# Performance work log

Hardware: AMD Instinct MI355X
Metric: run time of the kernel (lower is better)

The kernel has to match this reference:

```python
import jax, jax.numpy as jnp
import numpy as np
from jax import lax

B, T, H, W, C = 2, 16, 64, 64, 64
KT, K = 3, 3


def kernel_to_freq_3d(kernel, T, H, W):
    # kernel: (C, k_t, k_h, k_w) -> (C, T, H, W) complex freq response
    Cc, k_t, k_h, k_w = kernel.shape
    t_idx = (jnp.arange(k_t) - k_t // 2) % T
    h_idx = (jnp.arange(k_h) - k_h // 2) % H
    w_idx = (jnp.arange(k_w) - k_w // 2) % W
    tt, th, tw = jnp.meshgrid(t_idx, h_idx, w_idx, indexing='ij')
    padded = jnp.zeros((Cc, T, H, W), dtype=kernel.dtype).at[:, tt, th, tw].set(kernel)
    return jnp.fft.fftn(padded, axes=(1, 2, 3))


def mamba_op(left, right):
    a1, b1 = left
    a2, b2 = right
    return (a1 * a2, a2 * b1 + b2)


def setup_inputs() -> dict:
    key = jax.random.key(0)
    ks = jax.random.split(key, 8)
    fan_in = KT * K * K
    x = jax.random.normal(ks[0], (B, T, H, W, C), dtype=jnp.float32)
    A_kernel = jax.random.normal(ks[1], (C, KT, K, K), dtype=jnp.float32) / np.sqrt(fan_in)
    B_kernel = jax.random.normal(ks[2], (C, KT, K, K), dtype=jnp.float32) / np.sqrt(fan_in)
    forget_bias = jnp.full((C,), 2.0, dtype=jnp.float32)
    forget_scale = jnp.full((C,), 0.01, dtype=jnp.float32)
    input_bias = jnp.zeros((C,), dtype=jnp.float32)
    input_scale = jnp.full((C,), 0.01, dtype=jnp.float32)
    delta_W = jax.random.normal(ks[3], (C, C), dtype=jnp.float32) / np.sqrt(C)
    delta_b = jnp.zeros((C,), dtype=jnp.float32)
    return {"x": x, "A_kernel": A_kernel, "B_kernel": B_kernel,
            "forget_bias": forget_bias, "forget_scale": forget_scale,
            "input_bias": input_bias, "input_scale": input_scale,
            "delta_W": delta_W, "delta_b": delta_b}


def reference(x, A_kernel, B_kernel, forget_bias, forget_scale,
              input_bias, input_scale, delta_W, delta_b):
    Bb, Tt, Hh, Ww, Cc = x.shape
    # freq-domain kernels: (C,T,H,W) -> (T,1,H,W,C) for broadcasting over batch
    A_f = kernel_to_freq_3d(A_kernel, Tt, Hh, Ww).transpose(1, 2, 3, 0)[:, None]
    B_f = kernel_to_freq_3d(B_kernel, Tt, Hh, Ww).transpose(1, 2, 3, 0)[:, None]
    # input-dependent gates (real, elementwise per channel)
    forget_gate = jax.nn.sigmoid(forget_bias + forget_scale * x)
    input_gate = jax.nn.sigmoid(input_bias + input_scale * x)
    delta = jax.nn.softplus(jnp.einsum('bthwc,cd->bthwd', x, delta_W) + delta_b)
    x_f = jnp.fft.fftn(x, axes=(1, 2, 3))  # complex (B,T,H,W,C)
    # move time axis to front for the scan: (T,B,H,W,C)
    a_seq = forget_gate.transpose(1, 0, 2, 3, 4) * A_f
    b_seq = (input_gate.transpose(1, 0, 2, 3, 4)
             * delta.transpose(1, 0, 2, 3, 4)
             * B_f * x_f.transpose(1, 0, 2, 3, 4))
    _, h_all_f = lax.associative_scan(mamba_op, (a_seq, b_seq), axis=0)
    h_f = h_all_f.transpose(1, 0, 2, 3, 4)
    h = jnp.fft.ifftn(h_f, axes=(1, 2, 3)).real
    return h.astype(x.dtype)
```

## Files before the change

kernel.cpp:

```cpp
#include <hip/hip_runtime.h>
#include <math.h>

#define Bb 2
#define Tt 16
#define Hh 64
#define Ww 64
#define Cc 64
#define ST_ (Hh*Ww*Cc)
#define SB_ (Tt*Hh*Ww*Cc)

#define TWO_PI 6.2831853071795864769f

typedef __attribute__((ext_vector_type(8))) short bf16x8;
typedef __attribute__((ext_vector_type(4))) float f32x4;

#define BUF_A    0u
#define BUF_B    8388608u

__device__ __forceinline__ float2 cmul(float2 a, float2 b) {
    return make_float2(fmaf(a.x, b.x, -a.y * b.y), fmaf(a.x, b.y, a.y * b.x));
}
__device__ __forceinline__ float2 cadd(float2 a, float2 b) { return make_float2(a.x + b.x, a.y + b.y); }
__device__ __forceinline__ float2 csub(float2 a, float2 b) { return make_float2(a.x - b.x, a.y - b.y); }

__device__ __forceinline__ unsigned bfpack(float2 f) {
    unsigned r = __float_as_uint(f.x);
    unsigned i = __float_as_uint(f.y);
    r = (r + 0x7fffu + ((r >> 16) & 1u)) >> 16;
    i = (i + 0x7fffu + ((i >> 16) & 1u)) >> 16;
    return r | (i << 16);
}
__device__ __forceinline__ float2 bfunpack(unsigned u) {
    return make_float2(__uint_as_float(u << 16), __uint_as_float(u & 0xffff0000u));
}

union U48 { uint4 u4; uint2 u2[2]; unsigned u[4]; bf16x8 v8; };

__device__ __forceinline__ U48 tw_wf(int wp, int q, int ka, int reim) {
    U48 o;
#pragma unroll
    for (int p = 0; p < 4; ++p) {
        int k0 = ka * 32 + q * 8 + 2 * p;
        float v[2];
#pragma unroll
        for (int dk = 0; dk < 2; ++dk) {
            int k = k0 + dk;
            int a = (wp * k) & 63;
            float sn, cs; sincosf(TWO_PI * (float)a * (1.0f / 64.0f), &sn, &cs);
            v[dk] = reim ? -sn : cs;
        }
        o.u[p] = bfpack(make_float2(v[0], v[1]));
    }
    return o;
}

__device__ __forceinline__ U48 tw_cpx(int wp, int q, int ka, int reim, int tbl) {
    U48 o;
#pragma unroll
    for (int p = 0; p < 4; ++p) {
        int k0 = ka * 32 + q * 8 + 2 * p;
        float v[2];
#pragma unroll
        for (int dk = 0; dk < 2; ++dk) {
            int k = k0 + dk;
            int h = k >> 1;
            int a = (wp * h) & 63;
            float sn, cs; sincosf(TWO_PI * (float)a * (1.0f / 64.0f), &sn, &cs);
            bool even = (k & 1) == 0;
            float vv;
            if (tbl == 1) vv = reim ? (even ? -sn : cs) : (even ? cs : sn);
            else          vv = (reim ? (even ? sn : cs) : (even ? cs : -sn)) * (1.0f / 64.0f);
            v[dk] = vv;
        }
        o.u[p] = bfpack(make_float2(v[0], v[1]));
    }
    return o;
}

__device__ __forceinline__ U48 tw_wi(int wp, int q, int ka) {
    U48 o;
#pragma unroll
    for (int p = 0; p < 4; ++p) {
        int k0 = ka * 32 + q * 8 + 2 * p;
        float v[2];
#pragma unroll
        for (int dk = 0; dk < 2; ++dk) {
            int k = k0 + dk;
            int h = k >> 1;
            int a = (wp * h) & 63;
            float sn, cs; sincosf(TWO_PI * (float)a * (1.0f / 64.0f), &sn, &cs);
            bool even = (k & 1) == 0;
            v[dk] = (even ? cs : -sn) * (1.0f / 64.0f);
        }
        o.u[p] = bfpack(make_float2(v[0], v[1]));
    }
    return o;
}

__device__ __forceinline__ int zidx(int col, int h) {
    return (col << 6) + (h ^ (((col >> 1) & 7) << 3));
}

template <int S>
__device__ __forceinline__ void fft4(float2& a, float2& b, float2& c, float2& d) {
    float2 t0 = cadd(a, c), t1 = csub(a, c);
    float2 t2 = cadd(b, d), t3 = csub(b, d);
    a = cadd(t0, t2);
    c = csub(t0, t2);
    b = make_float2(t1.x - (float)S * t3.y, t1.y + (float)S * t3.x);
    d = make_float2(t1.x + (float)S * t3.y, t1.y - (float)S * t3.x);
}

template <int S>
__device__ __forceinline__ void fft16(float2 v[16]) {
    const float CS[10] = {1.f, 0.92387953f, 0.70710678f, 0.38268343f, 0.f,
                          -0.38268343f, -0.70710678f, -0.92387953f, -1.f, -0.92387953f};
    const float SN[10] = {0.f, 0.38268343f, 0.70710678f, 0.92387953f, 1.f,
                          0.92387953f, 0.70710678f, 0.38268343f, 0.f, -0.38268343f};
    float2 A[4][4];
#pragma unroll
    for (int j = 0; j < 4; ++j) {
        A[j][0] = v[j]; A[j][1] = v[4 + j]; A[j][2] = v[8 + j]; A[j][3] = v[12 + j];
        fft4<S>(A[j][0], A[j][1], A[j][2], A[j][3]);
#pragma unroll
        for (int k0 = 0; k0 < 4; ++k0) {
            int m = j * k0;
            float2 tw = make_float2(CS[m], (float)S * SN[m]);
            A[j][k0] = cmul(A[j][k0], tw);
        }
    }
#pragma unroll
    for (int k0 = 0; k0 < 4; ++k0) {
        fft4<S>(A[0][k0], A[1][k0], A[2][k0], A[3][k0]);
        v[k0] = A[0][k0]; v[k0 + 4] = A[1][k0]; v[k0 + 8] = A[2][k0]; v[k0 + 12] = A[3][k0];
    }
}

__global__ __launch_bounds__(512) void k_fwd2d(const float* __restrict__ x,
                                               unsigned* __restrict__ X2) {
    __shared__ unsigned Z[512 * 64];
    __shared__ unsigned P[8 * 16 * 32];
    int tid = threadIdx.x;
    int lane = tid & 63, r = (tid >> 6) & 3, team = tid >> 8;
    int wv = tid >> 6;
    int m = lane & 15, q = lane >> 4;
    int wg = blockIdx.x;
    int bt = wg >> 3;
    int c0 = (wg & 7) * 8;
    int b = wg >> 7, t = (wg >> 3) & 15;
    const float* xs = x + (size_t)bt * 262144;
    int wp = r * 16 + m;
    int hme = m >> 3, cme = m & 7;

    U48 Are[2], Aim[2];
#pragma unroll
    for (int ka = 0; ka < 2; ++ka) { Are[ka] = tw_wf(wp, q, ka, 0); Aim[ka] = tw_wf(wp, q, ka, 1); }

    int s_hl = lane >> 4;
    int s_p  = (lane >> 1) & 7;
    int s_cq = lane & 1;
    int s_hb = wv & 3;
    int s_wh = wv >> 2;

    for (int ch = 0; ch < 4; ++ch) {
        int hloc = s_hb * 4 + s_hl;
        int h = ch * 16 + hloc;
#pragma unroll
        for (int st = 0; st < 2; ++st) {
            int w2 = s_wh * 16 + st * 8 + s_p;
            const float* pa = xs + (size_t)h * 4096 + (size_t)w2 * 128 + (c0 + s_cq * 4);
            float4 f0 = *(const float4*)pa;
            float4 f1 = *(const float4*)(pa + 64);
            float a0[4] = {f0.x, f0.y, f0.z, f0.w};
            float a1[4] = {f1.x, f1.y, f1.z, f1.w};
            int hb3 = h & 3;
#pragma unroll
            for (int j = 0; j < 4; ++j) {
                int c = s_cq * 4 + j;
                int w2s = w2 ^ ((hb3 ^ ((c & 1) << 1)) << 3);
                P[c * 512 + hloc * 32 + w2s] = bfpack(make_float2(a0[j], a1[j]));
            }
        }
        __syncthreads();
#pragma unroll
        for (int gi = 0; gi < 4; ++gi) {
            int g = ch * 8 + gi * 2 + team;
            int h2 = g * 2 + hme;
            int hl2 = h2 & 15;
            int swz = ((h2 & 3) ^ ((cme & 1) << 1)) << 3;
            U48 B[2];
#pragma unroll
            for (int ka = 0; ka < 2; ++ka) {
                int w2a = (ka * 16 + q * 4) ^ swz;
                B[ka].u4 = *(const uint4*)&P[cme * 512 + hl2 * 32 + w2a];
            }
            f32x4 ar = {0.f, 0.f, 0.f, 0.f}, ai = {0.f, 0.f, 0.f, 0.f};
#pragma unroll
            for (int ka = 0; ka < 2; ++ka) {
                ar = __builtin_amdgcn_mfma_f32_16x16x32_bf16(Are[ka].v8, B[ka].v8, ar, 0, 0, 0);
                ai = __builtin_amdgcn_mfma_f32_16x16x32_bf16(Aim[ka].v8, B[ka].v8, ai, 0, 0, 0);
            }
#pragma unroll
            for (int reg = 0; reg < 4; ++reg) {
                int wpp = r * 16 + q * 4 + reg;
                Z[zidx(wpp * 8 + cme, h2)] = bfpack(make_float2(ar[reg], ai[reg]));
            }
        }
        __syncthreads();
    }

    U48 Hre[4], Him[4];
#pragma unroll
    for (int ka = 0; ka < 4; ++ka) { Hre[ka] = tw_cpx(wp, q, ka, 0, 1); Him[ka] = tw_cpx(wp, q, ka, 1, 1); }
    size_t ob = (size_t)b * 4194304 + (size_t)t * 64 + (c0 + cme);
#pragma unroll 2
    for (int gi = 0; gi < 16; ++gi) {
        int g = gi * 2 + team;
        int col = g * 16 + m;
        int w = g * 2 + hme;
        U48 B[4];
#pragma unroll
        for (int ka = 0; ka < 4; ++ka) {
            int h0 = ka * 16 + q * 4;
            int zi = zidx(col, h0);
            B[ka].u2[0] = *(const uint2*)&Z[zi];
            B[ka].u2[1] = *(const uint2*)&Z[zi + 2];
        }
        f32x4 ar = {0.f, 0.f, 0.f, 0.f}, ai = {0.f, 0.f, 0.f, 0.f};
#pragma unroll
        for (int ka = 0; ka < 4; ++ka) {
            ar = __builtin_amdgcn_mfma_f32_16x16x32_bf16(Hre[ka].v8, B[ka].v8, ar, 0, 0, 0);
            ai = __builtin_amdgcn_mfma_f32_16x16x32_bf16(Him[ka].v8, B[ka].v8, ai, 0, 0, 0);
        }
#pragma unroll
        for (int reg = 0; reg < 4; ++reg) {
            int hp = r * 16 + q * 4 + reg;
            X2[ob + (size_t)hp * 65536 + (size_t)w * 1024] = bfpack(make_float2(ar[reg], ai[reg]));
        }
    }
}

__global__ __launch_bounds__(512) void k_inv2d(const unsigned* __restrict__ X3,
                                               float* __restrict__ out) {
    __shared__ unsigned Z[512 * 64];
    __shared__ unsigned P[8 * 8 * 64];
    int tid = threadIdx.x;
    int lane = tid & 63, r = (tid >> 6) & 3, team = tid >> 8;
    int m = lane & 15, q = lane >> 4;
    int wg = blockIdx.x;
    int bt = wg >> 3;
    int c0 = (wg & 7) * 8;
    const unsigned* xs = X3 + (size_t)bt * 262144;
    int wp = r * 16 + m;
    int hme = m >> 3, cme = m & 7;

    U48 Hre[4], Him[4];
#pragma unroll
    for (int ka = 0; ka < 4; ++ka) { Hre[ka] = tw_cpx(wp, q, ka, 0, 2); Him[ka] = tw_cpx(wp, q, ka, 1, 2); }

    for (int cw = 0; cw < 8; ++cw) {
#pragma unroll
        for (int it = 0; it < 2; ++it) {
            int u = it * 512 + tid;
            int cq = u & 1, h = (u >> 1) & 63, wl = u >> 7;
            const unsigned* pa = xs + (size_t)(cw * 8 + wl) * 4096 + (size_t)h * 64 + (c0 + cq * 4);
            uint4 d = *(const uint4*)pa;
            unsigned dd[4] = {d.x, d.y, d.z, d.w};
#pragma unroll
            for (int j = 0; j < 4; ++j) {
                int c = cq * 4 + j;
                int hs = h ^ ((((wl & 3) ^ ((c & 1) << 1))) << 3);
                P[c * 512 + wl * 64 + hs] = dd[j];
            }
        }
        __syncthreads();
#pragma unroll
        for (int gi = 0; gi < 2; ++gi) {
            int g = cw * 4 + gi * 2 + team;
            int w = g * 2 + hme;
            int wl = w & 7;
            int swz = ((wl & 3) ^ ((cme & 1) << 1)) << 3;
            U48 B[4];
#pragma unroll
            for (int ka = 0; ka < 4; ++ka) {
                int ha = (ka * 16 + q * 4) ^ swz;
                B[ka].u4 = *(const uint4*)&P[cme * 512 + wl * 64 + ha];
            }
            f32x4 ar = {0.f, 0.f, 0.f, 0.f}, ai = {0.f, 0.f, 0.f, 0.f};
#pragma unroll
            for (int ka = 0; ka < 4; ++ka) {
                ar = __builtin_amdgcn_mfma_f32_16x16x32_bf16(Hre[ka].v8, B[ka].v8, ar, 0, 0, 0);
                ai = __builtin_amdgcn_mfma_f32_16x16x32_bf16(Him[ka].v8, B[ka].v8, ai, 0, 0, 0);
            }
#pragma unroll
            for (int reg = 0; reg < 4; ++reg) {
                int hp = r * 16 + q * 4 + reg;
                Z[zidx(hp * 8 + cme, w)] = bfpack(make_float2(ar[reg], ai[reg]));
            }
        }
        __syncthreads();
    }

    U48 Wre[4];
#pragma unroll
    for (int ka = 0; ka < 4; ++ka) Wre[ka] = tw_wi(wp, q, ka);
#pragma unroll 2
    for (int gi = 0; gi < 16; ++gi) {
        int g = gi * 2 + team;
        int col = g * 16 + m;
        int h = g * 2 + hme;
        U48 B[4];
#pragma unroll
        for (int ka = 0; ka < 4; ++ka) {
            int w0 = ka * 16 + q * 4;
            int zi = zidx(col, w0);
            B[ka].u2[0] = *(const uint2*)&Z[zi];
            B[ka].u2[1] = *(const uint2*)&Z[zi + 2];
        }
        f32x4 ar = {0.f, 0.f, 0.f, 0.f};
#pragma unroll
        for (int ka = 0; ka < 4; ++ka)
            ar = __builtin_amdgcn_mfma_f32_16x16x32_bf16(Wre[ka].v8, B[ka].v8, ar, 0, 0, 0);
        float* dst = out + (size_t)bt * 262144 + (size_t)h * 4096 + (c0 + cme);
#pragma unroll
        for (int reg = 0; reg < 4; ++reg) {
            int wpp = r * 16 + q * 4 + reg;
            dst[(size_t)wpp * 64] = ar[reg];
        }
    }
}

__global__ __launch_bounds__(256) void k_mid(
    const float* __restrict__ x, const unsigned* __restrict__ X2,
    unsigned* __restrict__ X3,
    const float* __restrict__ Ak, const float* __restrict__ Bk,
    const float* __restrict__ fb, const float* __restrict__ fs,
    const float* __restrict__ ib, const float* __restrict__ isc_,
    const float* __restrict__ dW, const float* __restrict__ db) {
    const float CT[16] = {1.f, 0.9238795f, 0.7071068f, 0.3826834f, 0.f, -0.3826834f,
                          -0.7071068f, -0.9238795f, -1.f, -0.9238795f, -0.7071068f,
                          -0.3826834f, 0.f, 0.3826834f, 0.7071068f, 0.9238795f};
    const float SN[16] = {0.f, 0.3826834f, 0.7071068f, 0.9238795f, 1.f, 0.9238795f,
                          0.7071068f, 0.3826834f, 0.f, -0.3826834f, -0.7071068f,
                          -0.9238795f, -1.f, -0.9238795f, -0.7071068f, -0.3826834f};
    __shared__ float Akl[1728], Bkl[1728];
    __shared__ __align__(16) float xs[4][16 * 68 + 4];

    int tid = threadIdx.x;
    int g = tid >> 6, lane = tid & 63;
    int c = lane;
    int m = lane & 15, q = lane >> 4;
    int site = blockIdx.x * 4 + g;
    int b = site >> 12, hw = site & 4095;
    int h = hw >> 6, w = hw & 63;
    size_t base = (size_t)b * SB_ + (size_t)hw * 64;

    for (int i = tid; i < 1728; i += 256) { Akl[i] = Ak[i]; Bkl[i] = Bk[i]; }

    U48 Ub[4][2];
#pragma unroll
    for (int nt = 0; nt < 4; ++nt)
#pragma unroll
        for (int ka = 0; ka < 2; ++ka)
#pragma unroll
            for (int p2 = 0; p2 < 4; ++p2) {
                int kb = ka * 32 + q * 8 + 2 * p2;
                int ccol = m + 16 * nt;
                Ub[nt][ka].u[p2] = bfpack(make_float2(dW[kb * 64 + ccol], dW[(kb + 1) * 64 + ccol]));
            }

    float xv[16];
    float2 v[16];
    const unsigned* src2 = X2 + (size_t)site * 1024;
#pragma unroll
    for (int t = 0; t < 16; ++t) {
        xv[t] = x[base + (size_t)t * ST_ + c];
        v[t] = bfunpack(src2[t * 64 + c]);
    }
#pragma unroll
    for (int t = 0; t < 16; ++t) xs[g][t * 68 + c] = xv[t];
    __syncthreads();

    bf16x8 Afrag[2];
#pragma unroll
    for (int ka = 0; ka < 2; ++ka) {
        int d0 = ka * 32 + q * 8;
        const float* p = &xs[g][m * 68 + d0];
        float4 f0 = *(const float4*)p;
        float4 f1 = *(const float4*)(p + 4);
        union { bf16x8 v8; unsigned uu[4]; } U;
        U.uu[0] = bfpack(make_float2(f0.x, f0.y));
        U.uu[1] = bfpack(make_float2(f0.z, f0.w));
        U.uu[2] = bfpack(make_float2(f1.x, f1.y));
        U.uu[3] = bfpack(make_float2(f1.z, f1.w));
        Afrag[ka] = U.v8;
    }
#pragma unroll
    for (int nt = 0; nt < 4; ++nt) {
        int ccol = m + 16 * nt;
        float dbn = db[ccol];
        f32x4 acc = {dbn, dbn, dbn, dbn};
#pragma unroll
        for (int ka = 0; ka < 2; ++ka)
            acc = __builtin_amdgcn_mfma_f32_16x16x32_bf16(Afrag[ka], Ub[nt][ka].v8, acc, 0, 0, 0);
#pragma unroll
        for (int reg = 0; reg < 4; ++reg)
            xs[g][(q * 4 + reg) * 68 + ccol] = acc[reg];
    }

    float sh, ch; sincosf(TWO_PI * (float)h / 64.0f, &sh, &ch);
    float sw, cw; sincosf(TWO_PI * (float)w / 64.0f, &sw, &cw);
    float2 eh[3] = { make_float2(ch, sh), make_float2(1.f, 0.f), make_float2(ch, -sh) };
    float2 ew[3] = { make_float2(cw, sw), make_float2(1.f, 0.f), make_float2(cw, -sw) };
    float2 GA[3], GB[3];
#pragma unroll
    for (int kt = 0; kt < 3; ++kt) { GA[kt] = make_float2(0.f, 0.f); GB[kt] = make_float2(0.f, 0.f); }
#pragma unroll
    for (int kh = 0; kh < 3; ++kh) {
#pragma unroll
        for (int kw = 0; kw < 3; ++kw) {
            float2 e = cmul(eh[kh], ew[kw]);
#pragma unroll
            for (int kt = 0; kt < 3; ++kt) {
                float ka = Akl[c * 27 + kt * 9 + kh * 3 + kw];
                float kb = Bkl[c * 27 + kt * 9 + kh * 3 + kw];
                GA[kt].x = fmaf(ka, e.x, GA[kt].x);
                GA[kt].y = fmaf(ka, e.y, GA[kt].y);
                GB[kt].x = fmaf(kb, e.x, GB[kt].x);
                GB[kt].y = fmaf(kb, e.y, GB[kt].y);
            }
        }
    }
    float fbc = fb[c], fsc = fs[c], ibc = ib[c], iscv = isc_[c];

    fft16<-1>(v);
    __syncthreads();

    float delta_raw[16];
#pragma unroll
    for (int t = 0; t < 16; ++t) delta_raw[t] = xs[g][t * 68 + c];

    float2 hv = make_float2(0.f, 0.f);
#pragma unroll
    for (int t = 0; t < 16; ++t) {
        float ct = CT[t], st = SN[t];
        float2 Af, Bf;
        Af.x = GA[1].x + ct * (GA[0].x + GA[2].x) - st * (GA[0].y - GA[2].y);
        Af.y = GA[1].y + ct * (GA[0].y + GA[2].y) + st * (GA[0].x - GA[2].x);
        Bf.x = GB[1].x + ct * (GB[0].x + GB[2].x) - st * (GB[0].y - GB[2].y);
        Bf.y = GB[1].y + ct * (GB[0].y + GB[2].y) + st * (GB[0].x - GB[2].x);

        float xc = xv[t];
        float fg  = __builtin_amdgcn_rcpf(1.f + __expf(-(fbc + fsc * xc)));
        float igv = __builtin_amdgcn_rcpf(1.f + __expf(-(ibc + iscv * xc)));
        float dot = delta_raw[t];
        float delta = (dot > 20.f) ? dot : __logf(1.f + __expf(dot));

        float sR = igv * delta;
        float2 bbv;
        bbv.x = sR * (Bf.x * v[t].x - Bf.y * v[t].y);
        bbv.y = sR * (Bf.x * v[t].y + Bf.y * v[t].x);
        float2 av = make_float2(fg * Af.x, fg * Af.y);
        float2 nh;
        nh.x = av.x * hv.x - av.y * hv.y + bbv.x;
        nh.y = av.x * hv.y + av.y * hv.x + bbv.y;
        hv = nh;
        v[t] = hv;
    }

    fft16<1>(v);

    size_t ob = (size_t)b * 4194304 + (size_t)w * 4096 + (size_t)h * 64 + c;
#pragma unroll
    for (int t = 0; t < 16; ++t) {
        float2 o = make_float2(v[t].x * 0.0625f, v[t].y * 0.0625f);
        X3[ob + (size_t)t * 262144] = bfpack(o);
    }
}

extern "C" void kernel_launch(void* const* d_in, const int* in_sizes, int n_in,
                              void* d_out, int out_size, void* d_ws, size_t ws_size,
                              hipStream_t stream) {
    const float* x   = (const float*)d_in[0];
    const float* Ak  = (const float*)d_in[1];
    const float* Bk  = (const float*)d_in[2];
    const float* fb  = (const float*)d_in[3];
    const float* fs  = (const float*)d_in[4];
    const float* ib  = (const float*)d_in[5];
    const float* is_ = (const float*)d_in[6];
    const float* dW  = (const float*)d_in[7];
    const float* db  = (const float*)d_in[8];
    float* out = (float*)d_out;
    unsigned* ws = (unsigned*)d_ws;
    unsigned* X2 = ws + BUF_A;
    unsigned* X3 = ws + BUF_B;

    k_fwd2d<<<Bb * Tt * 8, 512, 0, stream>>>(x, X2);
    k_mid<<<(Bb * Hh * Ww) / 4, 256, 0, stream>>>(x, X2, X3, Ak, Bk, fb, fs, ib, is_, dW, db);
    k_inv2d<<<Bb * Tt * 8, 512, 0, stream>>>(X3, out);
}
```

Baseline: 197.6 us.

## Halve channels per block in 2D FFT kernels and prefetch all global loads

Each block in the forward and inverse 2D FFT kernels now handles 4 channels instead of 8, which doubles the grid to 512 blocks and halves LDS use per block. The aim is more blocks resident per CU and better coverage of the GPU. Both kernels also issue every global load for a block into registers up front, then stage them into shared memory chunk by chunk, to hide memory latency. The cost is more register pressure from the prefetch buffers and twice as many per-block twiddle setups, with each global access now covering narrower contiguous segments.

```diff
diff --git a/kernel.cpp b/kernel.cpp
--- a/kernel.cpp
+++ b/kernel.cpp
@@ -136,56 +136,49 @@
     }
 }
 
-__global__ __launch_bounds__(512) void k_fwd2d(const float* __restrict__ x,
-                                               unsigned* __restrict__ X2) {
-    __shared__ unsigned Z[512 * 64];
-    __shared__ unsigned P[8 * 16 * 32];
+__global__ __launch_bounds__(512, 4) void k_fwd2d(const float* __restrict__ x,
+                                                  unsigned* __restrict__ X2) {
+    __shared__ unsigned Z[256 * 64];
+    __shared__ unsigned P[4 * 16 * 32];
     int tid = threadIdx.x;
     int lane = tid & 63, r = (tid >> 6) & 3, team = tid >> 8;
-    int wv = tid >> 6;
     int m = lane & 15, q = lane >> 4;
     int wg = blockIdx.x;
-    int bt = wg >> 3;
-    int c0 = (wg & 7) * 8;
-    int b = wg >> 7, t = (wg >> 3) & 15;
+    int bt = wg >> 4;
+    int c0 = (wg & 15) * 4;
+    int b = wg >> 8, t = (wg >> 4) & 15;
     const float* xs = x + (size_t)bt * 262144;
     int wp = r * 16 + m;
-    int hme = m >> 3, cme = m & 7;
+    int hme = m >> 2, cme = m & 3;
 
     U48 Are[2], Aim[2];
 #pragma unroll
     for (int ka = 0; ka < 2; ++ka) { Are[ka] = tw_wf(wp, q, ka, 0); Aim[ka] = tw_wf(wp, q, ka, 1); }
 
-    int s_hl = lane >> 4;
-    int s_p  = (lane >> 1) & 7;
-    int s_cq = lane & 1;
-    int s_hb = wv & 3;
-    int s_wh = wv >> 2;
-
+    int s_h = tid >> 5;
+    int s_w2 = tid & 31;
+    float4 f[4][2];
+#pragma unroll
     for (int ch = 0; ch < 4; ++ch) {
-        int hloc = s_hb * 4 + s_hl;
-        int h = ch * 16 + hloc;
-#pragma unroll
-        for (int st = 0; st < 2; ++st) {
-            int w2 = s_wh * 16 + st * 8 + s_p;
-            const float* pa = xs + (size_t)h * 4096 + (size_t)w2 * 128 + (c0 + s_cq * 4);
-            float4 f0 = *(const float4*)pa;
-            float4 f1 = *(const float4*)(pa + 64);
-            float a0[4] = {f0.x, f0.y, f0.z, f0.w};
-            float a1[4] = {f1.x, f1.y, f1.z, f1.w};
-            int hb3 = h & 3;
-#pragma unroll
-            for (int j = 0; j < 4; ++j) {
-                int c = s_cq * 4 + j;
-                int w2s = w2 ^ ((hb3 ^ ((c & 1) << 1)) << 3);
-                P[c * 512 + hloc * 32 + w2s] = bfpack(make_float2(a0[j], a1[j]));
-            }
+        const float* pa = xs + (size_t)(ch * 16 + s_h) * 4096 + (size_t)s_w2 * 128 + c0;
+        f[ch][0] = *(const float4*)pa;
+        f[ch][1] = *(const float4*)(pa + 64);
+    }
+
+    for (int ch = 0; ch < 4; ++ch) {
+        int h = ch * 16 + s_h;
+        float a0[4] = {f[ch][0].x, f[ch][0].y, f[ch][0].z, f[ch][0].w};
+        float a1[4] = {f[ch][1].x, f[ch][1].y, f[ch][1].z, f[ch][1].w};
+#pragma unroll
+        for (int j = 0; j < 4; ++j) {
+            int w2s = s_w2 ^ ((((h & 3) ^ ((j & 1) << 1))) << 3);
+            P[j * 512 + s_h * 32 + w2s] = bfpack(make_float2(a0[j], a1[j]));
         }
         __syncthreads();
 #pragma unroll
-        for (int gi = 0; gi < 4; ++gi) {
-            int g = ch * 8 + gi * 2 + team;
-            int h2 = g * 2 + hme;
+        for (int gi = 0; gi < 2; ++gi) {
+            int g = ch * 4 + gi * 2 + team;
+            int h2 = g * 4 + hme;
             int hl2 = h2 & 15;
             int swz = ((h2 & 3) ^ ((cme & 1) << 1)) << 3;
             U48 B[2];
@@ -203,7 +196,7 @@
 #pragma unroll
             for (int reg = 0; reg < 4; ++reg) {
                 int wpp = r * 16 + q * 4 + reg;
-                Z[zidx(wpp * 8 + cme, h2)] = bfpack(make_float2(ar[reg], ai[reg]));
+                Z[zidx(wpp * 4 + cme, h2)] = bfpack(make_float2(ar[reg], ai[reg]));
             }
         }
         __syncthreads();
@@ -214,10 +207,10 @@
     for (int ka = 0; ka < 4; ++ka) { Hre[ka] = tw_cpx(wp, q, ka, 0, 1); Him[ka] = tw_cpx(wp, q, ka, 1, 1); }
     size_t ob = (size_t)b * 4194304 + (size_t)t * 64 + (c0 + cme);
 #pragma unroll 2
-    for (int gi = 0; gi < 16; ++gi) {
+    for (int gi = 0; gi < 8; ++gi) {
         int g = gi * 2 + team;
         int col = g * 16 + m;
-        int w = g * 2 + hme;
+        int w = g * 4 + hme;
         U48 B[4];
 #pragma unroll
         for (int ka = 0; ka < 4; ++ka) {
@@ -240,44 +233,42 @@
     }
 }
 
-__global__ __launch_bounds__(512) void k_inv2d(const unsigned* __restrict__ X3,
-                                               float* __restrict__ out) {
-    __shared__ unsigned Z[512 * 64];
-    __shared__ unsigned P[8 * 8 * 64];
+__global__ __launch_bounds__(512, 4) void k_inv2d(const unsigned* __restrict__ X3,
+                                                  float* __restrict__ out) {
+    __shared__ unsigned Z[256 * 64];
+    __shared__ unsigned P[4 * 8 * 64];
     int tid = threadIdx.x;
     int lane = tid & 63, r = (tid >> 6) & 3, team = tid >> 8;
     int m = lane & 15, q = lane >> 4;
     int wg = blockIdx.x;
-    int bt = wg >> 3;
-    int c0 = (wg & 7) * 8;
+    int bt = wg >> 4;
+    int c0 = (wg & 15) * 4;
     const unsigned* xs = X3 + (size_t)bt * 262144;
     int wp = r * 16 + m;
-    int hme = m >> 3, cme = m & 7;
+    int hme = m >> 2, cme = m & 3;
 
     U48 Hre[4], Him[4];
 #pragma unroll
     for (int ka = 0; ka < 4; ++ka) { Hre[ka] = tw_cpx(wp, q, ka, 0, 2); Him[ka] = tw_cpx(wp, q, ka, 1, 2); }
 
+    int s_wl = tid >> 6;
+    int s_hh = tid & 63;
+    uint4 d[8];
+#pragma unroll
+    for (int cw = 0; cw < 8; ++cw)
+        d[cw] = *(const uint4*)(xs + (size_t)(cw * 8 + s_wl) * 4096 + (size_t)s_hh * 64 + c0);
+
     for (int cw = 0; cw < 8; ++cw) {
-#pragma unroll
-        for (int it = 0; it < 2; ++it) {
-            int u = it * 512 + tid;
-            int cq = u & 1, h = (u >> 1) & 63, wl = u >> 7;
-            const unsigned* pa = xs + (size_t)(cw * 8 + wl) * 4096 + (size_t)h * 64 + (c0 + cq * 4);
-            uint4 d = *(const uint4*)pa;
-            unsigned dd[4] = {d.x, d.y, d.z, d.w};
-#pragma unroll
-            for (int j = 0; j < 4; ++j) {
-                int c = cq * 4 + j;
-                int hs = h ^ ((((wl & 3) ^ ((c & 1) << 1))) << 3);
-                P[c * 512 + wl * 64 + hs] = dd[j];
-            }
+        unsigned dd[4] = {d[cw].x, d[cw].y, d[cw].z, d[cw].w};
+#pragma unroll
+        for (int j = 0; j < 4; ++j) {
+            int hs = s_hh ^ ((((s_wl & 3) ^ ((j & 1) << 1))) << 3);
+            P[j * 512 + s_wl * 64 + hs] = dd[j];
         }
         __syncthreads();
-#pragma unroll
-        for (int gi = 0; gi < 2; ++gi) {
-            int g = cw * 4 + gi * 2 + team;
-            int w = g * 2 + hme;
+        {
+            int g = cw * 2 + team;
+            int w = g * 4 + hme;
             int wl = w & 7;
             int swz = ((wl & 3) ^ ((cme & 1) << 1)) << 3;
             U48 B[4];
@@ -295,7 +286,7 @@
 #pragma unroll
             for (int reg = 0; reg < 4; ++reg) {
                 int hp = r * 16 + q * 4 + reg;
-                Z[zidx(hp * 8 + cme, w)] = bfpack(make_float2(ar[reg], ai[reg]));
+                Z[zidx(hp * 4 + cme, w)] = bfpack(make_float2(ar[reg], ai[reg]));
             }
         }
         __syncthreads();
@@ -305,10 +296,10 @@
 #pragma unroll
     for (int ka = 0; ka < 4; ++ka) Wre[ka] = tw_wi(wp, q, ka);
 #pragma unroll 2
-    for (int gi = 0; gi < 16; ++gi) {
+    for (int gi = 0; gi < 8; ++gi) {
         int g = gi * 2 + team;
         int col = g * 16 + m;
-        int h = g * 2 + hme;
+        int h = g * 4 + hme;
         U48 B[4];
 #pragma unroll
         for (int ka = 0; ka < 4; ++ka) {
@@ -495,7 +486,7 @@
     unsigned* X2 = ws + BUF_A;
     unsigned* X3 = ws + BUF_B;
 
-    k_fwd2d<<<Bb * Tt * 8, 512, 0, stream>>>(x, X2);
+    k_fwd2d<<<Bb * Tt * 16, 512, 0, stream>>>(x, X2);
     k_mid<<<(Bb * Hh * Ww) / 4, 256, 0, stream>>>(x, X2, X3, Ak, Bk, fb, fs, ib, is_, dW, db);
-    k_inv2d<<<Bb * Tt * 8, 512, 0, stream>>>(X3, out);
-}
+    k_inv2d<<<Bb * Tt * 16, 512, 0, stream>>>(X3, out);
+}
```

After: 252.2 us. 1.28x slower.
